# Kernel optimization log

Hardware: AMD Instinct MI355X
Metric: run time of the kernel (lower is better)

Reference implementation:

```python
import jax, jax.numpy as jnp
import numpy as np

NFRAMES, BS, LATENT = 196, 128, 1024
E = 16            # number of object types (experts)
NJOINTS = 128     # max joints -> padded width
NFEATS = 6
INPUT_FEATS = NJOINTS * NFEATS  # 768


def setup_inputs() -> dict:
    key = jax.random.key(0)
    k1, k2, k3, k4 = jax.random.split(key, 4)
    output = jax.random.normal(k1, (NFRAMES, BS, LATENT), dtype=jnp.float32)
    object_types = jax.random.randint(k2, (BS,), 0, E)
    # stacked per-type Linear params, zero-padded to INPUT_FEATS
    W = jax.random.normal(k3, (E, LATENT, INPUT_FEATS), dtype=jnp.float32) * (1.0 / np.sqrt(LATENT))
    b = jax.random.normal(k4, (E, INPUT_FEATS), dtype=jnp.float32) * 0.01
    # valid joints per type in [8, NJOINTS]
    joint_counts = jax.random.randint(jax.random.fold_in(key, 7), (E,), 8, NJOINTS + 1)
    return {"output": output, "object_types": object_types, "W": W, "b": b,
            "joint_counts": joint_counts}


def reference(output, object_types, W, b, joint_counts):
    # per-expert valid output width and column mask [E, INPUT_FEATS]
    feat_counts = joint_counts * NFEATS
    col_mask = (jnp.arange(INPUT_FEATS)[None, :] < feat_counts[:, None]).astype(output.dtype)
    # gather per-sample expert params: Wg [BS, LATENT, F], bg/mg [BS, F]
    Wg = W[object_types]
    bg = b[object_types]
    mg = col_mask[object_types]
    # y[t,b,f] = sum_d output[t,b,d] * Wg[b,d,f] + bg[b,f], zero-padded past valid width
    y = (jnp.einsum('tbd,bdf->tbf', output, Wg) + bg[None]) * mg[None]
    y = y.reshape(NFRAMES, BS, NJOINTS, NFEATS)
    return jnp.transpose(y, (1, 2, 3, 0))  # (bs, njoints, nfeats, nframes)
```

## Files before the change

kernel.cpp:

```cpp
#include <hip/hip_runtime.h>
#include <hip/hip_bf16.h>


#define NFRAMES 196
#define TPAD    208
#define BSZ     128
#define DLAT    1024
#define FIN     768
#define BM      128
#define BK      32
#define KSTEPS  (DLAT / BK)
#define MTILES  (FIN / BM)
#define NBLK    (MTILES * BSZ)
#define NTHREADS 256

typedef short bf16x8 __attribute__((ext_vector_type(8)));
typedef float f32x4  __attribute__((ext_vector_type(4)));
typedef unsigned int u32x2 __attribute__((ext_vector_type(2)));
typedef unsigned int u32x4 __attribute__((ext_vector_type(4)));

__device__ __forceinline__ unsigned int pkbf(float lo, float hi) {
    unsigned short a = (unsigned short)__builtin_bit_cast(short, __float2bfloat16(lo));
    unsigned short b = (unsigned short)__builtin_bit_cast(short, __float2bfloat16(hi));
    return (unsigned int)a | ((unsigned int)b << 16);
}

#define BAR() do { asm volatile("s_waitcnt lgkmcnt(0)" ::: "memory"); \
                   __builtin_amdgcn_s_barrier(); } while (0)

template<int NF>
__device__ __forceinline__ void mfma_all(const short* __restrict__ Bp, const int* idxB,
                                         const bf16x8 (&af)[4], f32x4 (&acc)[4][7]) {
    #pragma unroll
    for (int nf = 0; nf < NF; ++nf) {
        bf16x8 bv = *reinterpret_cast<const bf16x8*>(&Bp[idxB[nf]]);
        #pragma unroll
        for (int f = 0; f < 4; ++f)
            acc[f][nf] = __builtin_amdgcn_mfma_f32_16x16x32_bf16(af[f], bv, acc[f][nf], 0, 0, 0);
    }
}

template<int NF>
__device__ __forceinline__ void epilogue(const f32x4 (&acc)[4][7], float* __restrict__ outB,
                                         const float* __restrict__ biasE, int fcb, int m0,
                                         int wr, int wc, int g, int lr) {
    #pragma unroll
    for (int f = 0; f < 4; ++f) {
        #pragma unroll
        for (int rr = 0; rr < 4; ++rr) {
            const int fcol = m0 + wr * 64 + f * 16 + g * 4 + rr;
            const float bb = biasE[fcol];
            const bool  val = fcol < fcb;
            #pragma unroll
            for (int nf = 0; nf < NF; ++nf) {
                const int t = wc * 112 + nf * 16 + lr;
                if (t < NFRAMES)
                    outB[fcol * NFRAMES + t] = val ? (acc[f][nf][rr] + bb) : 0.f;
            }
        }
    }
}

__global__ __launch_bounds__(NTHREADS, 2)
void fused_expert_gemm(const float* __restrict__ X,
                       const int*   __restrict__ otypes,
                       const float* __restrict__ W,
                       const float* __restrict__ Bias,
                       const int*   __restrict__ jc,
                       float*       __restrict__ out)
{
    __shared__ short As[2][BM * BK];
    __shared__ short Bs[2][TPAD * BK];

    const int hw      = blockIdx.x;
    const int logical = (hw & 7) * (NBLK / 8) + (hw >> 3);
    const int b       = logical / MTILES;
    const int mt      = logical - b * MTILES;
    const int m0      = mt * BM;

    const int tid = threadIdx.x;
    const int e   = otypes[b];
    const int fcb = jc[e] * 6;
    float* outB = out + (size_t)b * (FIN * NFRAMES);

    if (m0 >= fcb) {
        f32x4 zz = {0.f, 0.f, 0.f, 0.f};
        f32x4* dst = reinterpret_cast<f32x4*>(outB + m0 * NFRAMES);
        const int total = (BM * NFRAMES) / 4;
        for (int i = tid; i < total; i += NTHREADS) dst[i] = zz;
        return;
    }

    const int wave = tid >> 6;
    const int lane = tid & 63;
    const int lr   = lane & 15;
    const int g    = lane >> 4;
    const int wr   = wave >> 1;
    const int wc   = wave & 1;

    const int mb  = tid & 31;
    const int kb  = tid >> 5;
    const int kbe = (kb + (mb >> 2)) & 7;
    const int ko = tid & 3;
    const int rw = tid >> 2;

    const f32x4* __restrict__ Xv = reinterpret_cast<const f32x4*>(X);
    const f32x4* __restrict__ Wv = reinterpret_cast<const f32x4*>(W);
    const f32x4 fz = {0.f, 0.f, 0.f, 0.f};

    f32x4 wa[4];
    f32x4 xb[4][2];

    int idxA[4], idxB[7];
    #pragma unroll
    for (int f = 0; f < 4; ++f)
        idxA[f] = (wr * 64 + f * 16 + lr) * BK + g * 8;
    #pragma unroll
    for (int nf = 0; nf < 7; ++nf)
        idxB[nf] = (wc * 112 + nf * 16 + lr) * BK + g * 8;

    f32x4 acc[4][7];
    #pragma unroll
    for (int f = 0; f < 4; ++f)
        #pragma unroll
        for (int nf = 0; nf < 7; ++nf) acc[f][nf] = fz;

    auto load_stage = [&](int kk) {
        #pragma unroll
        for (int i = 0; i < 4; ++i)
            wa[i] = Wv[(e * DLAT + kk + kbe * 4 + i) * (FIN / 4) + (m0 >> 2) + mb];
        #pragma unroll
        for (int p = 0; p < 4; ++p) {
            const int n = p * 64 + rw;
            if (n < NFRAMES) {
                const int base = (n * BSZ + b) * (DLAT / 4) + (kk >> 2) + ko * 2;
                xb[p][0] = Xv[base];
                xb[p][1] = Xv[base + 1];
            } else { xb[p][0] = fz; xb[p][1] = fz; }
        }
    };

    auto write_stage = [&](int buf) {
        #pragma unroll
        for (int jj = 0; jj < 4; ++jj) {
            const int r = (mb + jj) & 3;
            u32x2 v = { pkbf(wa[0][r], wa[1][r]), pkbf(wa[2][r], wa[3][r]) };
            *reinterpret_cast<u32x2*>(&As[buf][(mb * 4 + r) * BK + kbe * 4]) = v;
        }
        #pragma unroll
        for (int p = 0; p < 4; ++p) {
            const int n = p * 64 + rw;
            if (n < TPAD) {
                u32x4 v = { pkbf(xb[p][0][0], xb[p][0][1]), pkbf(xb[p][0][2], xb[p][0][3]),
                            pkbf(xb[p][1][0], xb[p][1][1]), pkbf(xb[p][1][2], xb[p][1][3]) };
                *reinterpret_cast<u32x4*>(&Bs[buf][n * BK + ko * 8]) = v;
            }
        }
    };

    load_stage(0);
    write_stage(0);
    load_stage(BK);
    BAR();

    #pragma unroll 1
    for (int j = 0; j < KSTEPS; ++j) {
        const int cur = j & 1;
        bf16x8 af[4];
        #pragma unroll
        for (int f = 0; f < 4; ++f)
            af[f] = *reinterpret_cast<const bf16x8*>(&As[cur][idxA[f]]);

        if (wc == 0) mfma_all<7>(Bs[cur], idxB, af, acc);
        else         mfma_all<6>(Bs[cur], idxB, af, acc);

        if (j + 1 < KSTEPS) write_stage(cur ^ 1);
        if (j + 2 < KSTEPS) load_stage((j + 2) * BK);
        BAR();
    }

    const float* biasE = Bias + e * FIN;
    if (wc == 0) epilogue<7>(acc, outB, biasE, fcb, m0, wr, wc, g, lr);
    else         epilogue<6>(acc, outB, biasE, fcb, m0, wr, wc, g, lr);
}

extern "C" void kernel_launch(void* const* d_in, const int* in_sizes, int n_in,
                              void* d_out, int out_size, void* d_ws, size_t ws_size,
                              hipStream_t stream) {
    const float* X    = (const float*)d_in[0];
    const int*   ot   = (const int*)d_in[1];
    const float* W    = (const float*)d_in[2];
    const float* Bias = (const float*)d_in[3];
    const int*   jc   = (const int*)d_in[4];
    float*       out  = (float*)d_out;

    dim3 grid(NBLK);
    dim3 block(NTHREADS);
    hipLaunchKernelGGL(fused_expert_gemm, grid, block, 0, stream,
                       X, ot, W, Bias, jc, out);
}
```

Measured before the change: 104.6 us.

## Use single-buffered LDS with two barriers per step and simple block mapping

Replaces the double-buffered LDS pipeline with one shared buffer. Each k-step now uses two barriers: wait, write the staged registers into LDS, prefetch the next global tile, wait again, then run the MFMAs. It also drops the XCD-aware block swizzle in favour of a direct mapping where blockIdx low bits select the batch and high bits select the M tile. This halves LDS use, which may raise occupancy, at the cost of an extra barrier per step, less overlap between LDS writes and MFMA, and different L2 locality.

After: 107.9 us. +3.1%, slower.

```diff
diff --git a/kernel.cpp b/kernel.cpp
--- a/kernel.cpp
+++ b/kernel.cpp
@@ -69,14 +69,13 @@
                        const int*   __restrict__ jc,
                        float*       __restrict__ out)
 {
-    __shared__ short As[2][BM * BK];
-    __shared__ short Bs[2][TPAD * BK];
+    __shared__ short As[BM * BK];
+    __shared__ short Bs[TPAD * BK];
 
-    const int hw      = blockIdx.x;
-    const int logical = (hw & 7) * (NBLK / 8) + (hw >> 3);
-    const int b       = logical / MTILES;
-    const int mt      = logical - b * MTILES;
-    const int m0      = mt * BM;
+    const int hw = blockIdx.x;
+    const int mt = hw >> 7;
+    const int b  = hw & 127;
+    const int m0 = mt * BM;
 
     const int tid = threadIdx.x;
     const int e   = otypes[b];
@@ -140,12 +139,12 @@
         }
     };
 
-    auto write_stage = [&](int buf) {
+    auto write_stage = [&]() {
         #pragma unroll
         for (int jj = 0; jj < 4; ++jj) {
             const int r = (mb + jj) & 3;
             u32x2 v = { pkbf(wa[0][r], wa[1][r]), pkbf(wa[2][r], wa[3][r]) };
-            *reinterpret_cast<u32x2*>(&As[buf][(mb * 4 + r) * BK + kbe * 4]) = v;
+            *reinterpret_cast<u32x2*>(&As[(mb * 4 + r) * BK + kbe * 4]) = v;
         }
         #pragma unroll
         for (int p = 0; p < 4; ++p) {
@@ -153,30 +152,27 @@
             if (n < TPAD) {
                 u32x4 v = { pkbf(xb[p][0][0], xb[p][0][1]), pkbf(xb[p][0][2], xb[p][0][3]),
                             pkbf(xb[p][1][0], xb[p][1][1]), pkbf(xb[p][1][2], xb[p][1][3]) };
-                *reinterpret_cast<u32x4*>(&Bs[buf][n * BK + ko * 8]) = v;
+                *reinterpret_cast<u32x4*>(&Bs[n * BK + ko * 8]) = v;
             }
         }
     };
 
     load_stage(0);
-    write_stage(0);
-    load_stage(BK);
-    BAR();
 
     #pragma unroll 1
-    for (int j = 0; j < KSTEPS; ++j) {
-        const int cur = j & 1;
+    for (int ks = 0; ks < KSTEPS; ++ks) {
+        BAR();
+        write_stage();
+        if (ks + 1 < KSTEPS)
+            load_stage((ks + 1) * BK);
+        BAR();
+
         bf16x8 af[4];
         #pragma unroll
         for (int f = 0; f < 4; ++f)
-            af[f] = *reinterpret_cast<const bf16x8*>(&As[cur][idxA[f]]);
-
-        if (wc == 0) mfma_all<7>(Bs[cur], idxB, af, acc);
-        else         mfma_all<6>(Bs[cur], idxB, af, acc);
-
-        if (j + 1 < KSTEPS) write_stage(cur ^ 1);
-        if (j + 2 < KSTEPS) load_stage((j + 2) * BK);
-        BAR();
+            af[f] = *reinterpret_cast<const bf16x8*>(&As[idxA[f]]);
+        if (wc == 0) mfma_all<7>(Bs, idxB, af, acc);
+        else         mfma_all<6>(Bs, idxB, af, acc);
     }
 
     const float* biasE = Bias + e * FIN;
```

## Stage X tile into LDS via direct global-to-LDS loads as fp32

Applied to the files above, without the earlier changes.

The activation (B) tile is now copied straight from global memory into shared memory with global_load_lds as fp32 in a swizzled layout, skipping register staging. The fp32-to-bf16 conversion moves into the compute step, which reads fp32 from LDS and packs it just before each MFMA. The A tile gets a padded pitch to cut bank conflicts, and the loop is reordered to issue next-stage loads before compute, draining vmcnt before each barrier. This trades less VGPR pressure and staging instructions for twice the LDS footprint and bandwidth on B, plus conversion work repeated per wave, which could lower occupancy.

Measured after the change: 212.6 us. 2.03x slower.

```diff
diff --git a/kernel.cpp b/kernel.cpp
--- a/kernel.cpp
+++ b/kernel.cpp
@@ -1,5 +1,6 @@
 #include <hip/hip_runtime.h>
 #include <hip/hip_bf16.h>
+#include <stdint.h>
 
 
 #define NFRAMES 196
@@ -13,6 +14,7 @@
 #define MTILES  (FIN / BM)
 #define NBLK    (MTILES * BSZ)
 #define NTHREADS 256
+#define A_PITCH 48
 
 typedef short bf16x8 __attribute__((ext_vector_type(8)));
 typedef float f32x4  __attribute__((ext_vector_type(4)));
@@ -25,15 +27,33 @@
     return (unsigned int)a | ((unsigned int)b << 16);
 }
 
+__device__ __forceinline__ void gload16(const float* g, float* lds) {
+    __builtin_amdgcn_global_load_lds(
+        (const __attribute__((address_space(1))) void*)g,
+        (__attribute__((address_space(3))) void*)lds,
+        16, 0, 0);
+}
+
+#define VMDRAIN() asm volatile("s_waitcnt vmcnt(0)" ::: "memory")
 #define BAR() do { asm volatile("s_waitcnt lgkmcnt(0)" ::: "memory"); \
                    __builtin_amdgcn_s_barrier(); } while (0)
 
 template<int NF>
-__device__ __forceinline__ void mfma_all(const short* __restrict__ Bp, const int* idxB,
-                                         const bf16x8 (&af)[4], f32x4 (&acc)[4][7]) {
+__device__ __forceinline__ void compute_step(const short* __restrict__ Ab,
+                                             const float* __restrict__ Bb,
+                                             const int* idxA, const int* ibase,
+                                             int c0, int c1, f32x4 (&acc)[4][7]) {
+    bf16x8 af[4];
+    #pragma unroll
+    for (int f = 0; f < 4; ++f)
+        af[f] = *reinterpret_cast<const bf16x8*>(&Ab[idxA[f]]);
     #pragma unroll
     for (int nf = 0; nf < NF; ++nf) {
-        bf16x8 bv = *reinterpret_cast<const bf16x8*>(&Bp[idxB[nf]]);
+        f32x4 q0 = *reinterpret_cast<const f32x4*>(&Bb[ibase[nf] + c0]);
+        f32x4 q1 = *reinterpret_cast<const f32x4*>(&Bb[ibase[nf] + c1]);
+        u32x4 u = { pkbf(q0[0], q0[1]), pkbf(q0[2], q0[3]),
+                    pkbf(q1[0], q1[1]), pkbf(q1[2], q1[3]) };
+        bf16x8 bv = __builtin_bit_cast(bf16x8, u);
         #pragma unroll
         for (int f = 0; f < 4; ++f)
             acc[f][nf] = __builtin_amdgcn_mfma_f32_16x16x32_bf16(af[f], bv, acc[f][nf], 0, 0, 0);
@@ -69,8 +89,8 @@
                        const int*   __restrict__ jc,
                        float*       __restrict__ out)
 {
-    __shared__ short As[2][BM * BK];
-    __shared__ short Bs[2][TPAD * BK];
+    __shared__ __align__(16) float Bsf[2][TPAD * BK];
+    __shared__ __align__(16) short As[2][BM * A_PITCH];
 
     const int hw      = blockIdx.x;
     const int logical = (hw & 7) * (NBLK / 8) + (hw >> 3);
@@ -98,84 +118,76 @@
     const int wr   = wave >> 1;
     const int wc   = wave & 1;
 
+    const int chunk = (lane & 7) ^ (lane >> 3);
+    const float* gbase[7];
+    #pragma unroll
+    for (int i = 0; i < 7; ++i) {
+        const int j = wave + 4 * i;
+        int n = j * 8 + (lane >> 3);
+        int t = n < NFRAMES ? n : NFRAMES - 1;
+        gbase[i] = X + (size_t)t * (BSZ * DLAT) + (size_t)b * DLAT + chunk * 4;
+    }
+
     const int mb  = tid & 31;
     const int kb  = tid >> 5;
     const int kbe = (kb + (mb >> 2)) & 7;
-    const int ko = tid & 3;
-    const int rw = tid >> 2;
-
-    const f32x4* __restrict__ Xv = reinterpret_cast<const f32x4*>(X);
     const f32x4* __restrict__ Wv = reinterpret_cast<const f32x4*>(W);
-    const f32x4 fz = {0.f, 0.f, 0.f, 0.f};
-
     f32x4 wa[4];
-    f32x4 xb[4][2];
-
-    int idxA[4], idxB[7];
+
+    int idxA[4], ibase[7];
     #pragma unroll
     for (int f = 0; f < 4; ++f)
-        idxA[f] = (wr * 64 + f * 16 + lr) * BK + g * 8;
+        idxA[f] = (wr * 64 + f * 16 + lr) * A_PITCH + g * 8;
     #pragma unroll
     for (int nf = 0; nf < 7; ++nf)
-        idxB[nf] = (wc * 112 + nf * 16 + lr) * BK + g * 8;
+        ibase[nf] = (wc * 112 + nf * 16 + lr) * BK;
+    const int c0 = ((2 * g) ^ (lr & 7)) * 4;
+    const int c1 = c0 ^ 4;
 
     f32x4 acc[4][7];
     #pragma unroll
     for (int f = 0; f < 4; ++f)
         #pragma unroll
-        for (int nf = 0; nf < 7; ++nf) acc[f][nf] = fz;
-
-    auto load_stage = [&](int kk) {
+        for (int nf = 0; nf < 7; ++nf) acc[f][nf] = {0.f, 0.f, 0.f, 0.f};
+
+    auto load_W = [&](int kk) {
         #pragma unroll
         for (int i = 0; i < 4; ++i)
             wa[i] = Wv[(e * DLAT + kk + kbe * 4 + i) * (FIN / 4) + (m0 >> 2) + mb];
-        #pragma unroll
-        for (int p = 0; p < 4; ++p) {
-            const int n = p * 64 + rw;
-            if (n < NFRAMES) {
-                const int base = (n * BSZ + b) * (DLAT / 4) + (kk >> 2) + ko * 2;
-                xb[p][0] = Xv[base];
-                xb[p][1] = Xv[base + 1];
-            } else { xb[p][0] = fz; xb[p][1] = fz; }
-        }
     };
-
-    auto write_stage = [&](int buf) {
+    auto write_A = [&](int buf) {
         #pragma unroll
         for (int jj = 0; jj < 4; ++jj) {
             const int r = (mb + jj) & 3;
             u32x2 v = { pkbf(wa[0][r], wa[1][r]), pkbf(wa[2][r], wa[3][r]) };
-            *reinterpret_cast<u32x2*>(&As[buf][(mb * 4 + r) * BK + kbe * 4]) = v;
-        }
-        #pragma unroll
-        for (int p = 0; p < 4; ++p) {
-            const int n = p * 64 + rw;
-            if (n < TPAD) {
-                u32x4 v = { pkbf(xb[p][0][0], xb[p][0][1]), pkbf(xb[p][0][2], xb[p][0][3]),
-                            pkbf(xb[p][1][0], xb[p][1][1]), pkbf(xb[p][1][2], xb[p][1][3]) };
-                *reinterpret_cast<u32x4*>(&Bs[buf][n * BK + ko * 8]) = v;
-            }
+            *reinterpret_cast<u32x2*>(&As[buf][(mb * 4 + r) * A_PITCH + kbe * 4]) = v;
         }
     };
-
-    load_stage(0);
-    write_stage(0);
-    load_stage(BK);
+    auto stage_B = [&](int buf, int koff) {
+        #pragma unroll
+        for (int i = 0; i < 6; ++i)
+            gload16(gbase[i] + koff, &Bsf[buf][(wave + 4 * i) * 256]);
+        if (wave < 2)
+            gload16(gbase[6] + koff, &Bsf[buf][(wave + 24) * 256]);
+    };
+
+    load_W(0);
+    write_A(0);
+    stage_B(0, 0);
+    load_W(BK);
+    VMDRAIN();
     BAR();
 
     #pragma unroll 1
-    for (int j = 0; j < KSTEPS; ++j) {
-        const int cur = j & 1;
-        bf16x8 af[4];
-        #pragma unroll
-        for (int f = 0; f < 4; ++f)
-            af[f] = *reinterpret_cast<const bf16x8*>(&As[cur][idxA[f]]);
-
-        if (wc == 0) mfma_all<7>(Bs[cur], idxB, af, acc);
-        else         mfma_all<6>(Bs[cur], idxB, af, acc);
-
-        if (j + 1 < KSTEPS) write_stage(cur ^ 1);
-        if (j + 2 < KSTEPS) load_stage((j + 2) * BK);
+    for (int ks = 0; ks < KSTEPS; ++ks) {
+        const int buf = ks & 1;
+        if (ks + 1 < KSTEPS) { write_A(buf ^ 1); stage_B(buf ^ 1, (ks + 1) * BK); }
+        if (ks + 2 < KSTEPS) load_W((ks + 2) * BK);
+
+        if (wc == 0) compute_step<7>(As[buf], Bsf[buf], idxA, ibase, c0, c1, acc);
+        else         compute_step<6>(As[buf], Bsf[buf], idxA, ibase, c0, c1, acc);
+
+        VMDRAIN();
         BAR();
     }
 
```
